# Kernel optimization log

Hardware: AMD Instinct MI355X
Metric: run time of the kernel (lower is better)

## Reference

```python
import jax, jax.numpy as jnp
import numpy as np


def setup_inputs() -> dict:
    key = jax.random.key(0)
    k1, k2, k3 = jax.random.split(key, 3)
    N, D, V = 16384, 256, 8192
    return {
        "z_real": jax.random.normal(k1, (N, D), jnp.float32),
        "z_imag": jax.random.normal(k2, (N, D), jnp.float32),
        "weight": jax.random.normal(k3, (V, 2 * D), jnp.float32) / np.sqrt(2 * D).astype(np.float32),
    }


def reference(z_real, z_imag, weight):
    sg = jax.lax.stop_gradient
    N, D = z_real.shape
    V = weight.shape[0]
    z_flat = jnp.concatenate([z_real, z_imag], axis=-1)  # (N, 2D)
    # Squared euclidean distance expansion; argmin over squared dist == argmin over cdist.
    x2 = jnp.sum(z_flat * z_flat, axis=-1, keepdims=True)            # (N, 1)
    w2 = jnp.sum(weight * weight, axis=-1)                           # (V,)
    d2 = x2 + w2[None, :] - 2.0 * jnp.einsum('nd,vd->nv', z_flat, weight)  # (N, V)
    indices = jnp.argmin(d2, axis=-1)                                # (N,)
    z_q = weight[indices]                                            # (N, 2D)
    # codebook loss + 0.25 * commitment loss, per-sample mean over feature dim
    loss_sample = jnp.mean((z_q - sg(z_flat)) ** 2, axis=-1) \
                + 0.25 * jnp.mean((sg(z_q) - z_flat) ** 2, axis=-1)  # (N,)
    # straight-through estimator
    z_q_st = z_flat + sg(z_q - z_flat)                               # (N, 2D)
    # entropy of empirical code usage (equivalent to one_hot(indices).mean(0))
    counts = jnp.zeros((V,), z_flat.dtype).at[indices].add(1.0)
    avg_probs = counts / jnp.asarray(N, z_flat.dtype)
    entropy = -jnp.sum(avg_probs * jnp.log(avg_probs + 1e-10))
    # split straight-through output back into real / imag halves (complex output)
    return z_q_st[..., :D], z_q_st[..., D:], loss_sample, indices, entropy
```

## Files before the change

kernel.cpp:

```cpp
#include <hip/hip_runtime.h>
#include <cmath>

typedef _Float16 half8 __attribute__((ext_vector_type(8)));
typedef float f32x4 __attribute__((ext_vector_type(4)));

constexpr int N = 16384;
constexpr int D = 256;
constexpr int K = 512;
constexpr int V = 8192;
constexpr float TAU = 0.015f;

#define GLOAD16(g, l) __builtin_amdgcn_global_load_lds(                     \
    (const __attribute__((address_space(1))) void*)(g),                    \
    (__attribute__((address_space(3))) void*)(l), 16, 0, 0)

__global__ __launch_bounds__(256) void vq_cvt(
    const float* __restrict__ zr, const float* __restrict__ zi,
    const float* __restrict__ w,
    _Float16* __restrict__ Zf, _Float16* __restrict__ Wf,
    double* __restrict__ w2d, float* __restrict__ w2f) {
  int t = blockIdx.x * 256 + threadIdx.x;
  if (t < N * 64) {
    int n = t >> 6, c8 = t & 63, k = c8 * 8;
    const float* src = (k < D) ? zr + (size_t)n * D + k : zi + (size_t)n * D + (k - D);
    float4 a = *(const float4*)src;
    float4 b = *(const float4*)(src + 4);
    half8 h;
    h[0] = (_Float16)a.x; h[1] = (_Float16)a.y; h[2] = (_Float16)a.z; h[3] = (_Float16)a.w;
    h[4] = (_Float16)b.x; h[5] = (_Float16)b.y; h[6] = (_Float16)b.z; h[7] = (_Float16)b.w;
    *(half8*)&Zf[(size_t)n * K + k] = h;
  } else {
    int t2 = t - N * 64;
    int vrow = t2 >> 6, c8 = t2 & 63, k = c8 * 8;
    const float* src = w + (size_t)vrow * K + k;
    float4 a = *(const float4*)src;
    float4 b = *(const float4*)(src + 4);
    half8 h;
    h[0] = (_Float16)a.x; h[1] = (_Float16)a.y; h[2] = (_Float16)a.z; h[3] = (_Float16)a.w;
    h[4] = (_Float16)b.x; h[5] = (_Float16)b.y; h[6] = (_Float16)b.z; h[7] = (_Float16)b.w;
    *(half8*)&Wf[(size_t)vrow * K + k] = h;
    double s = (double)a.x * a.x + (double)a.y * a.y + (double)a.z * a.z + (double)a.w * a.w +
               (double)b.x * b.x + (double)b.y * b.y + (double)b.z * b.z + (double)b.w * b.w;
#pragma unroll
    for (int off = 1; off < 64; off <<= 1) s += __shfl_xor(s, off, 64);
    if (c8 == 0) { w2d[vrow] = s; w2f[vrow] = (float)s; }
  }
}

__global__ __launch_bounds__(512) void vq_pass1(
    const _Float16* __restrict__ Zf, const _Float16* __restrict__ Wf,
    const float* __restrict__ w2f,
    float* __restrict__ pm1, float* __restrict__ pm2, int* __restrict__ pi1) {
  __shared__ __align__(16) unsigned short smem[3][12288];

  const int tid = threadIdx.x;
  const int w = tid >> 6, lane = tid & 63;
  const int wr = w >> 1, wc = w & 1;
  const int tx = lane & 15, g = lane >> 4;
  const int rsub = lane >> 2, kq = lane & 3;
  const int sbid = (blockIdx.x & 7) * 512 + (blockIdx.x >> 3);
  const int vt = sbid & 63, nt = sbid >> 6;
  const int rowBase = nt * 256, colBase = vt * 128;

  f32x4 acc[4][4];
#pragma unroll
  for (int m = 0; m < 4; ++m)
#pragma unroll
    for (int n = 0; n < 4; ++n) acc[m][n] = f32x4{0.f, 0.f, 0.f, 0.f};

  const int sst = (rsub >> 1) & 3;
  const int srd = (tx >> 1) & 3;

  const int zc0 = 2 * w, zc1 = 2 * w + 1;
  const int zrow0 = zc0 * 16 + rsub, zrow1 = zc1 * 16 + rsub;
  const int wrow = w * 16 + rsub;
  const int klane = ((kq ^ sst) << 3);

  const _Float16* z0 = Zf + (size_t)(rowBase + zrow0) * K + klane;
  const _Float16* z1 = Zf + (size_t)(rowBase + zrow1) * K + klane;
  const _Float16* w0 = Wf + (size_t)(colBase + wrow) * K + klane;

#define STAGE(buf, koff)                                                      \
  do {                                                                        \
    GLOAD16(z0 + (koff), &smem[buf][zc0 * 512]);                              \
    GLOAD16(z1 + (koff), &smem[buf][zc1 * 512]);                              \
    GLOAD16(w0 + (koff), &smem[buf][8192 + w * 512]);                         \
  } while (0)

  STAGE(0, 0);
  STAGE(1, 32);
  STAGE(2, 64);

#pragma unroll
  for (int t = 0; t < 16; ++t) {
    const int cur = t % 3;
    if (t <= 13)      asm volatile("s_waitcnt vmcnt(6)" ::: "memory");
    else if (t == 14) asm volatile("s_waitcnt vmcnt(3)" ::: "memory");
    else              asm volatile("s_waitcnt vmcnt(0)" ::: "memory");
    __builtin_amdgcn_s_barrier();

    half8 a[4], b[4];
#pragma unroll
    for (int m = 0; m < 4; ++m) {
      const int off = (wr * 64 + m * 16 + tx) * 32 + ((g ^ srd) << 3);
      a[m] = *(const half8*)&smem[cur][off];
    }
#pragma unroll
    for (int n = 0; n < 4; ++n) {
      const int off = 8192 + (wc * 64 + n * 16 + tx) * 32 + ((g ^ srd) << 3);
      b[n] = *(const half8*)&smem[cur][off];
    }
    __builtin_amdgcn_s_setprio(1);
#pragma unroll
    for (int m = 0; m < 4; ++m)
#pragma unroll
      for (int n = 0; n < 4; ++n)
        acc[m][n] = __builtin_amdgcn_mfma_f32_16x16x32_f16(a[m], b[n], acc[m][n], 0, 0, 0);
    __builtin_amdgcn_s_setprio(0);
    __builtin_amdgcn_s_barrier();
    if (t <= 12) STAGE(cur, (t + 3) * 32);
  }
#undef STAGE

  float wcol[4];
#pragma unroll
  for (int n = 0; n < 4; ++n) wcol[n] = w2f[colBase + wc * 64 + n * 16 + tx];
  const int cb = vt * 2 + wc;

#pragma unroll
  for (int m = 0; m < 4; ++m) {
#pragma unroll
    for (int r = 0; r < 4; ++r) {
      float m1 = 3.4e38f, m2 = 3.4e38f;
      int i1 = 0;
#pragma unroll
      for (int n = 0; n < 4; ++n) {
        float s = fmaf(-2.0f, acc[m][n][r], wcol[n]);
        if (s < m1) { m2 = m1; m1 = s; i1 = colBase + wc * 64 + n * 16 + tx; }
        else m2 = fminf(m2, s);
      }
#pragma unroll
      for (int off = 1; off < 16; off <<= 1) {
        float om1 = __shfl_xor(m1, off, 64);
        float om2 = __shfl_xor(m2, off, 64);
        int oi = __shfl_xor(i1, off, 64);
        float nm2 = fminf(fmaxf(m1, om1), fminf(m2, om2));
        if (om1 < m1 || (om1 == m1 && oi < i1)) { m1 = om1; i1 = oi; }
        m2 = nm2;
      }
      if (tx == 0) {
        int row = rowBase + wr * 64 + m * 16 + g * 4 + r;
        size_t o = (size_t)row * 128 + cb;
        pm1[o] = m1; pm2[o] = m2; pi1[o] = i1;
      }
    }
  }
}

__global__ __launch_bounds__(256) void vq_reduce(
    const float* __restrict__ pm1, const float* __restrict__ pm2,
    const int* __restrict__ pi1,
    float* __restrict__ out_idx, int* __restrict__ ws_idx,
    int* __restrict__ flaglist, int* __restrict__ nflag) {
  int row = blockIdx.x * 4 + (threadIdx.x >> 6);
  int lane = threadIdx.x & 63;
  size_t b = (size_t)row * 128;
  float a1 = pm1[b + lane], a2 = pm2[b + lane];
  int ai = pi1[b + lane];
  float b1 = pm1[b + lane + 64], b2 = pm2[b + lane + 64];
  int bi = pi1[b + lane + 64];
  float nm2 = fminf(fmaxf(a1, b1), fminf(a2, b2));
  if (b1 < a1 || (b1 == a1 && bi < ai)) { a1 = b1; ai = bi; }
  a2 = nm2;
#pragma unroll
  for (int off = 1; off < 64; off <<= 1) {
    float o1 = __shfl_xor(a1, off, 64);
    float o2 = __shfl_xor(a2, off, 64);
    int oi = __shfl_xor(ai, off, 64);
    float n2 = fminf(fmaxf(a1, o1), fminf(a2, o2));
    if (o1 < a1 || (o1 == a1 && oi < ai)) { a1 = o1; ai = oi; }
    a2 = n2;
  }
  if (lane == 0) {
    out_idx[row] = (float)ai;
    ws_idx[row] = ai;
    if (a2 - a1 < TAU) {
      int slot = atomicAdd(nflag, 1);
      flaglist[slot] = row;
    }
  }
}

__global__ __launch_bounds__(256) void vq_fixup(
    const float* __restrict__ zr, const float* __restrict__ zi,
    const float* __restrict__ w, const double* __restrict__ w2d,
    const float* __restrict__ pm1, const float* __restrict__ pm2,
    const int* __restrict__ pi1,
    const int* __restrict__ flaglist, const int* __restrict__ nflag,
    float* __restrict__ out_idx, int* __restrict__ ws_idx) {
  __shared__ float zrow[K];
  __shared__ float redf[128];
  __shared__ int slist[128];
  __shared__ int hlist[128];
  __shared__ int ns_s, nh_s;
  __shared__ float thr_s;
  __shared__ double wmin[4];
  __shared__ int widx[4];
  const int tid = threadIdx.x;
  const int lane = tid & 63, wvq = tid >> 6;
  const int nf = *nflag;

  for (int f = blockIdx.x; f < nf; f += gridDim.x) {
    const int row = flaglist[f];
    __syncthreads();
    if (tid == 0) { ns_s = 0; nh_s = 0; }
    zrow[tid] = zr[(size_t)row * D + tid];
    zrow[256 + tid] = zi[(size_t)row * D + tid];
    if (tid < 128) redf[tid] = pm1[(size_t)row * 128 + tid];
    __syncthreads();
    if (wvq == 0) {
      float v = fminf(redf[lane], redf[lane + 64]);
#pragma unroll
      for (int off = 1; off < 64; off <<= 1) v = fminf(v, __shfl_xor(v, off, 64));
      if (lane == 0) thr_s = v + TAU;
    }
    __syncthreads();
    const float thr = thr_s;
    if (tid < 128) {
      if (pm2[(size_t)row * 128 + tid] <= thr) {
        hlist[atomicAdd(&nh_s, 1)] = tid;
      } else if (redf[tid] <= thr) {
        slist[atomicAdd(&ns_s, 1)] = pi1[(size_t)row * 128 + tid];
      }
    }
    __syncthreads();
    const int ns = ns_s, nh = nh_s;

    double best = 1e300;
    int bi = 0x7fffffff;

    for (int ci = tid >> 3; ci < ns; ci += 32) {
      const int code = slist[ci], sub = tid & 7;
      const float4* w4 = (const float4*)(w + (size_t)code * K + sub * 64);
      const float4* z4 = (const float4*)(zrow + sub * 64);
      double d0 = 0.0, d1 = 0.0;
#pragma unroll
      for (int k4 = 0; k4 < 16; k4 += 2) {
        float4 a0 = w4[k4], b0 = z4[k4];
        float4 a1 = w4[k4 + 1], b1 = z4[k4 + 1];
        d0 = fma((double)a0.x, (double)b0.x, d0); d0 = fma((double)a0.y, (double)b0.y, d0);
        d0 = fma((double)a0.z, (double)b0.z, d0); d0 = fma((double)a0.w, (double)b0.w, d0);
        d1 = fma((double)a1.x, (double)b1.x, d1); d1 = fma((double)a1.y, (double)b1.y, d1);
        d1 = fma((double)a1.z, (double)b1.z, d1); d1 = fma((double)a1.w, (double)b1.w, d1);
      }
      double dot = d0 + d1;
      dot += __shfl_xor(dot, 1, 64);
      dot += __shfl_xor(dot, 2, 64);
      dot += __shfl_xor(dot, 4, 64);
      if (sub == 0) {
        double d = w2d[code] - 2.0 * dot;
        if (d < best || (d == best && code < bi)) { best = d; bi = code; }
      }
    }

    for (int hi = wvq; hi < nh; hi += 4) {
      const int code = hlist[hi] * 64 + lane;
      const float4* w4 = (const float4*)(w + (size_t)code * K);
      const float4* z4 = (const float4*)zrow;
      double d0 = 0.0, d1 = 0.0, d2 = 0.0, d3 = 0.0;
      for (int k4 = 0; k4 < 128; k4 += 4) {
        float4 a0 = w4[k4], b0 = z4[k4];
        float4 a1 = w4[k4 + 1], b1 = z4[k4 + 1];
        float4 a2 = w4[k4 + 2], b2 = z4[k4 + 2];
        float4 a3 = w4[k4 + 3], b3 = z4[k4 + 3];
        d0 = fma((double)a0.x, (double)b0.x, d0); d0 = fma((double)a0.y, (double)b0.y, d0);
        d0 = fma((double)a0.z, (double)b0.z, d0); d0 = fma((double)a0.w, (double)b0.w, d0);
        d1 = fma((double)a1.x, (double)b1.x, d1); d1 = fma((double)a1.y, (double)b1.y, d1);
        d1 = fma((double)a1.z, (double)b1.z, d1); d1 = fma((double)a1.w, (double)b1.w, d1);
        d2 = fma((double)a2.x, (double)b2.x, d2); d2 = fma((double)a2.y, (double)b2.y, d2);
        d2 = fma((double)a2.z, (double)b2.z, d2); d2 = fma((double)a2.w, (double)b2.w, d2);
        d3 = fma((double)a3.x, (double)b3.x, d3); d3 = fma((double)a3.y, (double)b3.y, d3);
        d3 = fma((double)a3.z, (double)b3.z, d3); d3 = fma((double)a3.w, (double)b3.w, d3);
      }
      double d = w2d[code] - 2.0 * ((d0 + d1) + (d2 + d3));
      if (d < best || (d == best && code < bi)) { best = d; bi = code; }
    }

#pragma unroll
    for (int off = 1; off < 64; off <<= 1) {
      double ob = __shfl_xor(best, off, 64);
      int oi = __shfl_xor(bi, off, 64);
      if (ob < best || (ob == best && oi < bi)) { best = ob; bi = oi; }
    }
    if (lane == 0) { wmin[wvq] = best; widx[wvq] = bi; }
    __syncthreads();
    if (tid == 0) {
      double b0 = wmin[0]; int i0 = widx[0];
      for (int q = 1; q < 4; ++q)
        if (wmin[q] < b0 || (wmin[q] == b0 && widx[q] < i0)) { b0 = wmin[q]; i0 = widx[q]; }
      out_idx[row] = (float)i0;
      ws_idx[row] = i0;
    }
  }
}

__global__ __launch_bounds__(256) void vq_gather(
    const float* __restrict__ zr, const float* __restrict__ zi,
    const float* __restrict__ w, const int* __restrict__ ws_idx,
    float* __restrict__ out0, float* __restrict__ out1,
    float* __restrict__ out2, unsigned int* __restrict__ counts) {
  int row = blockIdx.x * 4 + (threadIdx.x >> 6);
  int lane = threadIdx.x & 63;
  int idx = ws_idx[row];
  const float4* wr = (const float4*)(w + (size_t)idx * K);
  float4 q0 = wr[lane];
  float4 q1 = wr[64 + lane];
  float4 a = ((const float4*)(zr + (size_t)row * D))[lane];
  float4 b = ((const float4*)(zi + (size_t)row * D))[lane];
  ((float4*)(out0 + (size_t)row * D))[lane] = q0;
  ((float4*)(out1 + (size_t)row * D))[lane] = q1;

  float s = 0.f, dx;
  dx = q0.x - a.x; s = fmaf(dx, dx, s);
  dx = q0.y - a.y; s = fmaf(dx, dx, s);
  dx = q0.z - a.z; s = fmaf(dx, dx, s);
  dx = q0.w - a.w; s = fmaf(dx, dx, s);
  dx = q1.x - b.x; s = fmaf(dx, dx, s);
  dx = q1.y - b.y; s = fmaf(dx, dx, s);
  dx = q1.z - b.z; s = fmaf(dx, dx, s);
  dx = q1.w - b.w; s = fmaf(dx, dx, s);
#pragma unroll
  for (int off = 1; off < 64; off <<= 1) s += __shfl_xor(s, off, 64);
  if (lane == 0) {
    out2[row] = s * (1.25f / 512.f);
    atomicAdd(counts + idx, 1u);
  }
}

__global__ __launch_bounds__(256) void vq_entropy(const unsigned int* __restrict__ counts,
                                                  float* __restrict__ out4) {
  __shared__ double sd[256];
  int tid = threadIdx.x;
  double e = 0.0;
  for (int v = tid; v < V; v += 256) {
    double p = (double)counts[v] * (1.0 / (double)N);
    e += p * log(p + 1e-10);
  }
  sd[tid] = e;
  __syncthreads();
  for (int s = 128; s > 0; s >>= 1) {
    if (tid < s) sd[tid] += sd[tid + s];
    __syncthreads();
  }
  if (tid == 0) *out4 = -(float)sd[0];
}

extern "C" void kernel_launch(void* const* d_in, const int* in_sizes, int n_in,
                              void* d_out, int out_size, void* d_ws, size_t ws_size,
                              hipStream_t stream) {
  const float* zr = (const float*)d_in[0];
  const float* zi = (const float*)d_in[1];
  const float* w = (const float*)d_in[2];

  float* out = (float*)d_out;
  float* out0 = out;
  float* out1 = out + (size_t)N * D;
  float* out2 = out + (size_t)2 * N * D;
  float* out3 = out2 + N;
  float* out4 = out3 + N;

  float* pm1 = out;
  float* pm2 = out + (size_t)N * 128;
  int* pi1 = (int*)(out + (size_t)2 * N * 128);

  char* ws = (char*)d_ws;
  _Float16* Zf = (_Float16*)ws;
  _Float16* Wf = (_Float16*)(ws + (((size_t)16) << 20));
  char* ws2 = ws + (((size_t)24) << 20);
  double* w2d = (double*)ws2;
  float* w2f = (float*)(ws2 + 65536);
  unsigned int* counts = (unsigned int*)(ws2 + 98304);
  int* ws_idx = (int*)(ws2 + 131072);
  int* flaglist = (int*)(ws2 + 196608);
  int* nflag = (int*)(ws2 + 262144);

  (void)hipMemsetAsync(counts, 0, V * sizeof(unsigned int), stream);
  (void)hipMemsetAsync(nflag, 0, sizeof(int), stream);

  vq_cvt<<<(N * 64 + V * 64) / 256, 256, 0, stream>>>(zr, zi, w, Zf, Wf, w2d, w2f);
  vq_pass1<<<(N / 256) * (V / 128), 512, 0, stream>>>(Zf, Wf, w2f, pm1, pm2, pi1);
  vq_reduce<<<N / 4, 256, 0, stream>>>(pm1, pm2, pi1, out3, ws_idx, flaglist, nflag);
  vq_fixup<<<4096, 256, 0, stream>>>(zr, zi, w, w2d, pm1, pm2, pi1, flaglist, nflag,
                                     out3, ws_idx);
  vq_gather<<<N / 4, 256, 0, stream>>>(zr, zi, w, ws_idx, out0, out1, out2, counts);
  vq_entropy<<<1, 256, 0, stream>>>(counts, out4);
}
```

Baseline: 294.9 us.

## Load codebook operand straight to registers and shrink LDS for two blocks per CU

The codebook (B) tiles for the distance GEMM now come straight from global memory into registers with inline global_load_dwordx4, issued one k-step ahead. Only the Z tiles still go through the triple-buffered LDS. This cuts the LDS footprint from three 24 KB buffers to three 16 KB ones, and launch_bounds(512,2) asks for two resident blocks per CU to gain occupancy and drop the B LDS round-trip. In exchange, waves sharing a column tile load the same W data from global/L1 separately. The hand-written vmcnt waits and barriers are intricate and could under-synchronise the Z LDS reads.

New measurement: 381.8 us (median of 3 runs). 1.29x slower.

```diff
diff --git a/kernel.cpp b/kernel.cpp
--- a/kernel.cpp
+++ b/kernel.cpp
@@ -47,11 +47,11 @@
   }
 }
 
-__global__ __launch_bounds__(512) void vq_pass1(
+__global__ __launch_bounds__(512, 2) void vq_pass1(
     const _Float16* __restrict__ Zf, const _Float16* __restrict__ Wf,
     const float* __restrict__ w2f,
     float* __restrict__ pm1, float* __restrict__ pm2, int* __restrict__ pi1) {
-  __shared__ __align__(16) unsigned short smem[3][12288];
+  __shared__ __align__(16) unsigned short smem[3][8192];
 
   const int tid = threadIdx.x;
   const int w = tid >> 6, lane = tid & 63;
@@ -73,54 +73,65 @@
 
   const int zc0 = 2 * w, zc1 = 2 * w + 1;
   const int zrow0 = zc0 * 16 + rsub, zrow1 = zc1 * 16 + rsub;
-  const int wrow = w * 16 + rsub;
   const int klane = ((kq ^ sst) << 3);
-
   const _Float16* z0 = Zf + (size_t)(rowBase + zrow0) * K + klane;
   const _Float16* z1 = Zf + (size_t)(rowBase + zrow1) * K + klane;
-  const _Float16* w0 = Wf + (size_t)(colBase + wrow) * K + klane;
-
-#define STAGE(buf, koff)                                                      \
-  do {                                                                        \
+
+  const _Float16* ba0 = Wf + (size_t)(colBase + wc * 64 + 0 * 16 + tx) * K + g * 8;
+  const _Float16* ba1 = Wf + (size_t)(colBase + wc * 64 + 1 * 16 + tx) * K + g * 8;
+  const _Float16* ba2 = Wf + (size_t)(colBase + wc * 64 + 2 * 16 + tx) * K + g * 8;
+  const _Float16* ba3 = Wf + (size_t)(colBase + wc * 64 + 3 * 16 + tx) * K + g * 8;
+
+  half8 b0, b1, b2, b3;
+#define BLOADS() do {                                                         \
+    asm volatile("global_load_dwordx4 %0, %1, off" : "=v"(b0) : "v"(ba0) : "memory"); \
+    asm volatile("global_load_dwordx4 %0, %1, off" : "=v"(b1) : "v"(ba1) : "memory"); \
+    asm volatile("global_load_dwordx4 %0, %1, off" : "=v"(b2) : "v"(ba2) : "memory"); \
+    asm volatile("global_load_dwordx4 %0, %1, off" : "=v"(b3) : "v"(ba3) : "memory"); \
+    ba0 += 32; ba1 += 32; ba2 += 32; ba3 += 32;                               \
+  } while (0)
+#define STAGE_Z(buf, koff) do {                                               \
     GLOAD16(z0 + (koff), &smem[buf][zc0 * 512]);                              \
     GLOAD16(z1 + (koff), &smem[buf][zc1 * 512]);                              \
-    GLOAD16(w0 + (koff), &smem[buf][8192 + w * 512]);                         \
   } while (0)
 
-  STAGE(0, 0);
-  STAGE(1, 32);
-  STAGE(2, 64);
+  BLOADS();
+  STAGE_Z(0, 0); STAGE_Z(1, 32); STAGE_Z(2, 64);
+  asm volatile("s_waitcnt vmcnt(4)" ::: "memory");
+  __builtin_amdgcn_s_barrier();
 
 #pragma unroll
   for (int t = 0; t < 16; ++t) {
     const int cur = t % 3;
-    if (t <= 13)      asm volatile("s_waitcnt vmcnt(6)" ::: "memory");
-    else if (t == 14) asm volatile("s_waitcnt vmcnt(3)" ::: "memory");
-    else              asm volatile("s_waitcnt vmcnt(0)" ::: "memory");
-    __builtin_amdgcn_s_barrier();
-
-    half8 a[4], b[4];
+    half8 a[4];
 #pragma unroll
     for (int m = 0; m < 4; ++m) {
       const int off = (wr * 64 + m * 16 + tx) * 32 + ((g ^ srd) << 3);
       a[m] = *(const half8*)&smem[cur][off];
     }
-#pragma unroll
-    for (int n = 0; n < 4; ++n) {
-      const int off = 8192 + (wc * 64 + n * 16 + tx) * 32 + ((g ^ srd) << 3);
-      b[n] = *(const half8*)&smem[cur][off];
+    if (t >= 1 && t <= 13) {
+      asm volatile("s_waitcnt vmcnt(2)" ::: "memory");
+      __builtin_amdgcn_sched_barrier(0);
+    } else if (t >= 14) {
+      asm volatile("s_waitcnt vmcnt(0)" ::: "memory");
+      __builtin_amdgcn_sched_barrier(0);
     }
     __builtin_amdgcn_s_setprio(1);
 #pragma unroll
-    for (int m = 0; m < 4; ++m)
-#pragma unroll
-      for (int n = 0; n < 4; ++n)
-        acc[m][n] = __builtin_amdgcn_mfma_f32_16x16x32_f16(a[m], b[n], acc[m][n], 0, 0, 0);
+    for (int m = 0; m < 4; ++m) {
+      acc[m][0] = __builtin_amdgcn_mfma_f32_16x16x32_f16(a[m], b0, acc[m][0], 0, 0, 0);
+      acc[m][1] = __builtin_amdgcn_mfma_f32_16x16x32_f16(a[m], b1, acc[m][1], 0, 0, 0);
+      acc[m][2] = __builtin_amdgcn_mfma_f32_16x16x32_f16(a[m], b2, acc[m][2], 0, 0, 0);
+      acc[m][3] = __builtin_amdgcn_mfma_f32_16x16x32_f16(a[m], b3, acc[m][3], 0, 0, 0);
+    }
     __builtin_amdgcn_s_setprio(0);
+    if (t < 15) BLOADS();
+    if (t == 0) asm volatile("s_waitcnt vmcnt(6)" ::: "memory");
     __builtin_amdgcn_s_barrier();
-    if (t <= 12) STAGE(cur, (t + 3) * 32);
-  }
-#undef STAGE
+    if (t <= 12) STAGE_Z(cur, (t + 3) * 32);
+  }
+#undef BLOADS
+#undef STAGE_Z
 
   float wcol[4];
 #pragma unroll
```
